# Optimization experiments

Hardware: AMD Instinct MI355X
Metric: run time of the kernel (lower is better)

The kernel has to match this reference:

```python
import math
import jax, jax.numpy as jnp
import numpy as np

RCR = 5.2   # radial cutoff
RCA = 3.5   # angular cutoff
B, N, T, KR, KA = 256, 24, 4, 16, 32

# static index tables (depend only on N)
_NIDX = np.array([[j for j in range(N) if j != i] for i in range(N)])  # [N, N-1] neighbors excluding self
_I1, _I2 = np.triu_indices(N - 1, k=1)                                  # pair combinations, P = C(N-1,2)


def setup_inputs() -> dict:
    key = jax.random.key(0)
    k1, k2 = jax.random.split(key)
    coords = jax.random.normal(k1, (B, N, 3), dtype=jnp.float32)
    atom_types = jax.random.randint(k2, (N,), 0, T)
    EtaR = jnp.full((T, KR), 16.0, dtype=jnp.float32)
    ShfR = jnp.tile(jnp.linspace(0.9, 4.95, KR, dtype=jnp.float32), (T, 1))
    Zeta = jnp.full((T, KA), 32.0, dtype=jnp.float32)
    ShfZ = jnp.tile(jnp.tile(jnp.linspace(0.9, 3.525, 8, dtype=jnp.float32), 4), (T, 1))
    EtaA = jnp.full((T, KA), 8.0, dtype=jnp.float32)
    ShfA = jnp.tile(jnp.repeat(jnp.linspace(0.3927, 2.7489, 4, dtype=jnp.float32), 8), (T, 1))
    return dict(coords=coords, atom_types=atom_types, EtaR=EtaR, ShfR=ShfR,
                Zeta=Zeta, ShfZ=ShfZ, EtaA=EtaA, ShfA=ShfA)


def reference(coords, atom_types, EtaR, ShfR, Zeta, ShfZ, EtaA, ShfA):
    # pairwise vectors excluding self: rij[b,i,k] = coords[b,i] - coords[b, j_k], j_k != i
    rij = coords[:, :, None, :] - coords[:, _NIDX, :]                      # [B,N,N-1,3]

    # gather per-atom parameter rows: [N, K] -> broadcast as [1,N,1,K]
    etaR = EtaR[atom_types][None, :, None, :]
    shfR = ShfR[atom_types][None, :, None, :]
    zeta = Zeta[atom_types][None, :, None, :]
    shfZ = ShfZ[atom_types][None, :, None, :]
    etaA = EtaA[atom_types][None, :, None, :]
    shfA = ShfA[atom_types][None, :, None, :]

    # ---- radial G2 ----
    dij = jnp.linalg.norm(rij, axis=3)                                     # [B,N,N-1]
    fij = 0.5 * (jnp.cos(dij * (math.pi / RCR)) + 1.0)
    g2 = jnp.sum(jnp.exp(-etaR * (dij[..., None] - shfR) ** 2) * fij[..., None], axis=2)  # [B,N,KR]

    # ---- angular G3 (ANI) ----
    r12 = rij[:, :, _I1]                                                   # [B,N,P,3]
    r13 = rij[:, :, _I2]
    d12 = jnp.linalg.norm(r12, axis=3)                                     # [B,N,P]
    d13 = jnp.linalg.norm(r13, axis=3)
    f12 = 0.5 * (jnp.cos(d12 * (math.pi / RCA)) + 1.0)
    f13 = 0.5 * (jnp.cos(d13 * (math.pi / RCA)) + 1.0)
    cosine = jnp.einsum('bnpc,bnpc->bnp', r12, r13) / (d12 * d13)
    cosine = jnp.clip(cosine, -1.0 + 1e-7, 1.0 - 1e-7)  # numerical guard for acos
    cosang = jnp.cos(jnp.arccos(cosine)[..., None] - shfA)                 # [B,N,P,KA]
    g3 = jnp.sum(
        2.0 ** (1.0 - zeta) * (1.0 + cosang) ** zeta
        * jnp.exp(-etaA * (0.5 * (d12 + d13)[..., None] - shfZ) ** 2)
        * (f12 * f13)[..., None],
        axis=2)                                                            # [B,N,KA]

    return jnp.concatenate((g2, g3), axis=2)                               # [B,N,KR+KA]
```

## Files before the change

kernel.cpp:

```cpp
#include <hip/hip_runtime.h>


constexpr int CB = 256;
constexpr int CN = 24;
constexpr int CKR = 16;
constexpr int CKA = 32;
constexpr int NN = 23;
constexpr int NP = 253;
constexpr int NPpad = 256;
constexpr int KOUT = CKR + CKA;
#define LOG2E 1.44269504088896340736f

template<int MASK, int BIT, int HALF>
__device__ inline void red_level(float* acc, int lane) {
    const bool hi = (lane >> BIT) & 1;
#pragma unroll
    for (int j = 0; j < HALF; ++j) {
        float send = hi ? acc[j] : acc[j + HALF];
        float recv = __shfl_xor(send, MASK, 64);
        float keep = hi ? acc[j + HALF] : acc[j];
        acc[j] = keep + recv;
    }
}

__global__ __launch_bounds__(256) void ani_kernel(
    const float* __restrict__ coords, const int* __restrict__ atom_types,
    const float* __restrict__ EtaR, const float* __restrict__ ShfR,
    const float* __restrict__ Zeta, const float* __restrict__ ShfZ,
    const float* __restrict__ EtaA, const float* __restrict__ ShfA,
    float* __restrict__ out)
{
    __shared__ float s_rx[4][NN], s_ry[4][NN], s_rz[4][NN];
    __shared__ float s_d [4][NN], s_inv[4][NN], s_fA[4][NN], s_fR[4][NN];
    __shared__ unsigned char s_pa[NP], s_pb[NP];
    __shared__ float4 s_pair[4][NPpad];

    const int wv   = threadIdx.x >> 6;
    const int lane = threadIdx.x & 63;
    const int row  = blockIdx.x * 4 + wv;
    const int b    = row / CN;
    const int i    = row - b * CN;

    for (int p = threadIdx.x; p < NP; p += 256) {
        int a = 0, pp = p;
        while (pp >= (NN - 1 - a)) { pp -= (NN - 1 - a); ++a; }
        s_pa[p] = (unsigned char)a;
        s_pb[p] = (unsigned char)(a + 1 + pp);
    }

    const float cix = coords[row*3+0], ciy = coords[row*3+1], ciz = coords[row*3+2];
    if (lane < NN) {
        const int j   = lane + (lane >= i ? 1 : 0);
        const int idx = (b * CN + j) * 3;
        const float dx = cix - coords[idx+0];
        const float dy = ciy - coords[idx+1];
        const float dz = ciz - coords[idx+2];
        const float d  = __builtin_amdgcn_sqrtf(dx*dx + dy*dy + dz*dz);
        s_rx[wv][lane] = dx; s_ry[wv][lane] = dy; s_rz[wv][lane] = dz;
        s_d  [wv][lane] = d;
        s_inv[wv][lane] = __builtin_amdgcn_rcpf(d);
        s_fR[wv][lane] = 0.5f * (__cosf(d * (float)(3.14159265358979323846/5.2)) + 1.0f);
        s_fA[wv][lane] = 0.5f * (__cosf(d * (float)(3.14159265358979323846/3.5)) + 1.0f);
    }
    __syncthreads();

    #pragma unroll
    for (int it = 0; it < 4; ++it) {
        const int p = lane + it * 64;
        if (p < NP) {
            const int a = s_pa[p], c = s_pb[p];
            const float d12 = s_d[wv][a], d13 = s_d[wv][c];
            const float dot = s_rx[wv][a]*s_rx[wv][c]
                            + s_ry[wv][a]*s_ry[wv][c]
                            + s_rz[wv][a]*s_rz[wv][c];
            float cosv = dot * (s_inv[wv][a] * s_inv[wv][c]);
            cosv = fminf(fmaxf(cosv, -1.0f + 1e-7f), 1.0f - 1e-7f);
            const float sinv = __builtin_amdgcn_sqrtf(1.0f - cosv * cosv);
            const float avg  = 0.5f * (d12 + d13);
            const float ff2  = 2.0f * s_fA[wv][a] * s_fA[wv][c];
            s_pair[wv][p] = make_float4(cosv, sinv, avg, ff2);
        } else {
            s_pair[wv][p] = make_float4(0.0f, 0.0f, 0.0f, 0.0f);
        }
    }

    const int t = atom_types[i];

    {
        const int k = lane & 15, g = lane >> 4;
        const float eta = EtaR[t*CKR + k] * LOG2E;
        const float shf = ShfR[t*CKR + k];
        float acc = 0.0f;
        for (int j = g; j < NN; j += 4) {
            const float x = s_d[wv][j] - shf;
            acc += __builtin_amdgcn_exp2f(-eta * x * x) * s_fR[wv][j];
        }
        acc += __shfl_xor(acc, 16, 64);
        acc += __shfl_xor(acc, 32, 64);
        if (lane < CKR) out[row * KOUT + k] = acc;
    }

    __syncthreads();

    const float* __restrict__ Zt = ShfZ + t*CKA;
    const float* __restrict__ At = ShfA + t*CKA;
    const int kk = lane & 31;
    const bool okl = (Zeta[t*CKA + kk] == 32.0f)
                  && (EtaA[t*CKA + kk] == EtaA[t*CKA])
                  && (Zt[kk] == Zt[kk & 7])
                  && (At[kk] == At[kk & 24]);
    const bool fast = __all(okl);

    if (fast) {
        const float cgau = -EtaA[t*CKA] * LOG2E;
        float Zv[8], cAv[4], sAv[4];
        #pragma unroll
        for (int z = 0; z < 8; ++z) Zv[z] = Zt[z];
        #pragma unroll
        for (int a = 0; a < 4; ++a) {
            const float sh = At[a * 8];
            cAv[a] = __cosf(sh); sAv[a] = __sinf(sh);
        }
        float acc[32];
        #pragma unroll
        for (int k = 0; k < 32; ++k) acc[k] = 0.0f;

        const float4* __restrict__ prow = &s_pair[wv][0];
        #pragma unroll
        for (int it = 0; it < 4; ++it) {
            const float4 pd = prow[lane + it * 64];
            float G[8];
            #pragma unroll
            for (int z = 0; z < 8; ++z) {
                const float x = pd.z - Zv[z];
                G[z] = __builtin_amdgcn_exp2f(cgau * x * x);
            }
            #pragma unroll
            for (int a = 0; a < 4; ++a) {
                const float cosang = pd.x * cAv[a] + pd.y * sAv[a];
                const float hh  = 0.5f * cosang + 0.5f;
                const float h2 = hh*hh, h4 = h2*h2, h8 = h4*h4, h16 = h8*h8;
                const float Pa = (h16 * h16) * pd.w;
                #pragma unroll
                for (int z = 0; z < 8; ++z)
                    acc[a*8 + z] = fmaf(Pa, G[z], acc[a*8 + z]);
            }
        }

        red_level<1, 0, 16>(acc, lane);
        red_level<2, 1,  8>(acc, lane);
        red_level<4, 2,  4>(acc, lane);
        red_level<8, 3,  2>(acc, lane);
        red_level<16, 4, 1>(acc, lane);
        acc[0] += __shfl_xor(acc[0], 32, 64);
        if (lane < 32) {
            const int k = ((lane & 1) << 4) | ((lane & 2) << 2) | (lane & 4)
                        | ((lane & 8) >> 2) | ((lane & 16) >> 4);
            out[row * KOUT + CKR + k] = acc[0];
        }
    } else {
        const int k = lane & 31, h = lane >> 5;
        const float zeta  = Zeta[t*CKA + k];
        const float shfZ  = Zt[k];
        const float etaAl = EtaA[t*CKA + k] * LOG2E;
        const float shfA  = At[k];
        const float cA = __cosf(shfA), sA = __sinf(shfA);
        const float4* __restrict__ prow = &s_pair[wv][0];
        float acc = 0.0f;
        int p = h;
        #pragma unroll 4
        for (int it = 0; it < 127; ++it) {
            const float4 pd = prow[p]; p += 2;
            const float cosang = pd.x * cA + pd.y * sA;
            const float hh  = 0.5f * cosang + 0.5f;
            const float l2h = __log2f(hh);
            const float x   = pd.z - shfZ;
            const float e   = zeta * l2h - etaAl * x * x;
            acc += pd.w * __builtin_amdgcn_exp2f(e);
        }
        acc += __shfl_xor(acc, 32, 64);
        if (lane < CKA) out[row * KOUT + CKR + k] = acc;
    }
}

extern "C" void kernel_launch(void* const* d_in, const int* in_sizes, int n_in,
                              void* d_out, int out_size, void* d_ws, size_t ws_size,
                              hipStream_t stream) {
    const float* coords     = (const float*)d_in[0];
    const int*   atom_types = (const int*)  d_in[1];
    const float* EtaR       = (const float*)d_in[2];
    const float* ShfR       = (const float*)d_in[3];
    const float* Zeta       = (const float*)d_in[4];
    const float* ShfZ       = (const float*)d_in[5];
    const float* EtaA       = (const float*)d_in[6];
    const float* ShfA       = (const float*)d_in[7];
    float* out = (float*)d_out;

    dim3 grid((CB * CN) / 4), block(256);
    hipLaunchKernelGGL(ani_kernel, grid, block, 0, stream,
                       coords, atom_types, EtaR, ShfR, Zeta, ShfZ, EtaA, ShfA, out);
}
```

Baseline: 78.84 us.

## Keep pair features in registers and move pair index table to constant memory

Pair index tables are built at compile time in constant memory instead of being computed per block in shared memory. Each lane now holds its four pair feature vectors in registers rather than staging them through a shared float4 buffer. The block-wide syncthreads calls are replaced by a wave barrier, since each wave only uses its own shared rows. The fallback path now recomputes pair features inline, and the fast path holds 16 more registers per lane.

```diff
diff --git a/kernel.cpp b/kernel.cpp
--- a/kernel.cpp
+++ b/kernel.cpp
@@ -7,9 +7,21 @@
 constexpr int CKA = 32;
 constexpr int NN = 23;
 constexpr int NP = 253;
-constexpr int NPpad = 256;
 constexpr int KOUT = CKR + CKA;
 #define LOG2E 1.44269504088896340736f
+
+struct PairTab { unsigned char pa[256]; unsigned char pb[256]; };
+static constexpr PairTab make_pairs() {
+    PairTab t{};
+    int p = 0;
+    for (int i = 0; i < NN; ++i)
+        for (int j = i + 1; j < NN; ++j) {
+            t.pa[p] = (unsigned char)i; t.pb[p] = (unsigned char)j; ++p;
+        }
+    for (; p < 256; ++p) { t.pa[p] = 0; t.pb[p] = 0; }
+    return t;
+}
+__constant__ PairTab cPairs = make_pairs();
 
 template<int MASK, int BIT, int HALF>
 __device__ inline void red_level(float* acc, int lane) {
@@ -32,21 +44,12 @@
 {
     __shared__ float s_rx[4][NN], s_ry[4][NN], s_rz[4][NN];
     __shared__ float s_d [4][NN], s_inv[4][NN], s_fA[4][NN], s_fR[4][NN];
-    __shared__ unsigned char s_pa[NP], s_pb[NP];
-    __shared__ float4 s_pair[4][NPpad];
 
     const int wv   = threadIdx.x >> 6;
     const int lane = threadIdx.x & 63;
     const int row  = blockIdx.x * 4 + wv;
     const int b    = row / CN;
     const int i    = row - b * CN;
-
-    for (int p = threadIdx.x; p < NP; p += 256) {
-        int a = 0, pp = p;
-        while (pp >= (NN - 1 - a)) { pp -= (NN - 1 - a); ++a; }
-        s_pa[p] = (unsigned char)a;
-        s_pb[p] = (unsigned char)(a + 1 + pp);
-    }
 
     const float cix = coords[row*3+0], ciy = coords[row*3+1], ciz = coords[row*3+2];
     if (lane < NN) {
@@ -62,27 +65,7 @@
         s_fR[wv][lane] = 0.5f * (__cosf(d * (float)(3.14159265358979323846/5.2)) + 1.0f);
         s_fA[wv][lane] = 0.5f * (__cosf(d * (float)(3.14159265358979323846/3.5)) + 1.0f);
     }
-    __syncthreads();
-
-    #pragma unroll
-    for (int it = 0; it < 4; ++it) {
-        const int p = lane + it * 64;
-        if (p < NP) {
-            const int a = s_pa[p], c = s_pb[p];
-            const float d12 = s_d[wv][a], d13 = s_d[wv][c];
-            const float dot = s_rx[wv][a]*s_rx[wv][c]
-                            + s_ry[wv][a]*s_ry[wv][c]
-                            + s_rz[wv][a]*s_rz[wv][c];
-            float cosv = dot * (s_inv[wv][a] * s_inv[wv][c]);
-            cosv = fminf(fmaxf(cosv, -1.0f + 1e-7f), 1.0f - 1e-7f);
-            const float sinv = __builtin_amdgcn_sqrtf(1.0f - cosv * cosv);
-            const float avg  = 0.5f * (d12 + d13);
-            const float ff2  = 2.0f * s_fA[wv][a] * s_fA[wv][c];
-            s_pair[wv][p] = make_float4(cosv, sinv, avg, ff2);
-        } else {
-            s_pair[wv][p] = make_float4(0.0f, 0.0f, 0.0f, 0.0f);
-        }
-    }
+    __builtin_amdgcn_wave_barrier();
 
     const int t = atom_types[i];
 
@@ -100,7 +83,22 @@
         if (lane < CKR) out[row * KOUT + k] = acc;
     }
 
-    __syncthreads();
+    float4 pd[4];
+    #pragma unroll
+    for (int it = 0; it < 4; ++it) {
+        const int p = lane + it * 64;
+        const int a = cPairs.pa[p], c = cPairs.pb[p];
+        const float d12 = s_d[wv][a], d13 = s_d[wv][c];
+        const float dot = s_rx[wv][a]*s_rx[wv][c]
+                        + s_ry[wv][a]*s_ry[wv][c]
+                        + s_rz[wv][a]*s_rz[wv][c];
+        float cosv = dot * (s_inv[wv][a] * s_inv[wv][c]);
+        cosv = fminf(fmaxf(cosv, -1.0f + 1e-7f), 1.0f - 1e-7f);
+        const float sinv = __builtin_amdgcn_sqrtf(1.0f - cosv * cosv);
+        const float avg  = 0.5f * (d12 + d13);
+        const float ff2  = (p < NP) ? 2.0f * s_fA[wv][a] * s_fA[wv][c] : 0.0f;
+        pd[it] = make_float4(cosv, sinv, avg, ff2);
+    }
 
     const float* __restrict__ Zt = ShfZ + t*CKA;
     const float* __restrict__ At = ShfA + t*CKA;
@@ -125,22 +123,21 @@
         #pragma unroll
         for (int k = 0; k < 32; ++k) acc[k] = 0.0f;
 
-        const float4* __restrict__ prow = &s_pair[wv][0];
         #pragma unroll
         for (int it = 0; it < 4; ++it) {
-            const float4 pd = prow[lane + it * 64];
+            const float4 q = pd[it];
             float G[8];
             #pragma unroll
             for (int z = 0; z < 8; ++z) {
-                const float x = pd.z - Zv[z];
+                const float x = q.z - Zv[z];
                 G[z] = __builtin_amdgcn_exp2f(cgau * x * x);
             }
             #pragma unroll
             for (int a = 0; a < 4; ++a) {
-                const float cosang = pd.x * cAv[a] + pd.y * sAv[a];
+                const float cosang = q.x * cAv[a] + q.y * sAv[a];
                 const float hh  = 0.5f * cosang + 0.5f;
                 const float h2 = hh*hh, h4 = h2*h2, h8 = h4*h4, h16 = h8*h8;
-                const float Pa = (h16 * h16) * pd.w;
+                const float Pa = (h16 * h16) * q.w;
                 #pragma unroll
                 for (int z = 0; z < 8; ++z)
                     acc[a*8 + z] = fmaf(Pa, G[z], acc[a*8 + z]);
@@ -165,18 +162,22 @@
         const float etaAl = EtaA[t*CKA + k] * LOG2E;
         const float shfA  = At[k];
         const float cA = __cosf(shfA), sA = __sinf(shfA);
-        const float4* __restrict__ prow = &s_pair[wv][0];
         float acc = 0.0f;
-        int p = h;
-        #pragma unroll 4
-        for (int it = 0; it < 127; ++it) {
-            const float4 pd = prow[p]; p += 2;
-            const float cosang = pd.x * cA + pd.y * sA;
+        for (int p = h; p < NP; p += 2) {
+            const int a = cPairs.pa[p], c = cPairs.pb[p];
+            const float d12 = s_d[wv][a], d13 = s_d[wv][c];
+            const float dot = s_rx[wv][a]*s_rx[wv][c]
+                            + s_ry[wv][a]*s_ry[wv][c]
+                            + s_rz[wv][a]*s_rz[wv][c];
+            float cosv = dot * (s_inv[wv][a] * s_inv[wv][c]);
+            cosv = fminf(fmaxf(cosv, -1.0f + 1e-7f), 1.0f - 1e-7f);
+            const float sinv = __builtin_amdgcn_sqrtf(1.0f - cosv * cosv);
+            const float cosang = cosv * cA + sinv * sA;
             const float hh  = 0.5f * cosang + 0.5f;
             const float l2h = __log2f(hh);
-            const float x   = pd.z - shfZ;
+            const float x   = 0.5f * (d12 + d13) - shfZ;
             const float e   = zeta * l2h - etaAl * x * x;
-            acc += pd.w * __builtin_amdgcn_exp2f(e);
+            acc += (2.0f * s_fA[wv][a] * s_fA[wv][c]) * __builtin_amdgcn_exp2f(e);
         }
         acc += __shfl_xor(acc, 32, 64);
         if (lane < CKA) out[row * KOUT + CKR + k] = acc;
```

Result: no change. 78.58 us (-0.3%).
